# Optimization experiments

Measured on AMD Instinct MI355X. Metric: run time of the kernel, lower is better.

## Reference

```python
import jax, jax.numpy as jnp
import numpy as np


def setup_inputs() -> dict:
    key = jax.random.key(0)
    k0, k1, k2, k3 = jax.random.split(key, 4)
    B, H, W, C, h = 2, 64, 64, 256, 8
    N = H * W
    # per-pixel, per-head (dy, dx) match offsets; a few pixels of displacement
    max_offset = jax.random.normal(k0, (B, N, h, 2), dtype=jnp.float32) * 4.0
    q = jax.random.normal(k1, (B, N, C), dtype=jnp.float32)
    k = jax.random.normal(k2, (B, N, C), dtype=jnp.float32)
    v = jax.random.normal(k3, (B, N, C), dtype=jnp.float32)
    return {"max_offset": max_offset, "q": q, "k": k, "v": v,
            "H": H, "W": W, "r_h": 3, "r_w": 3}


def reference(max_offset, q, k, v, H, W, r_h, r_w):
    """MatchAttention fused forward (l1_norm, scale=1.0).

    Each query pixel (y,x), head g attends to a (2*r_h+1)x(2*r_w+1) window
    centered at (y,x) + round(max_offset[...,g]), clamped to the image.
    Similarity is the negative L1 distance between q and gathered k.
    Returns (output [B,N,C], attn_out [B,N,h,K]).
    """
    B, N, C = q.shape
    h = max_offset.shape[2]
    Ch = C // h
    scale = 1.0
    attn_type = "l1_norm"  # fixed; 'l2_norm' would use squared distance

    # window deltas, K = (2*r_h+1)*(2*r_w+1)
    dy = jnp.arange(-r_h, r_h + 1)
    dx = jnp.arange(-r_w, r_w + 1)
    gy, gx = jnp.meshgrid(dy, dx, indexing="ij")
    ddy, ddx = gy.reshape(-1), gx.reshape(-1)  # [K]

    ys = (jnp.arange(N) // W)[None, :, None]  # [1,N,1]
    xs = (jnp.arange(N) % W)[None, :, None]

    off = jnp.round(max_offset).astype(jnp.int32)  # [B,N,h,2] (dy,dx)
    cy = ys + off[..., 0]                          # [B,N,h] window center
    cx = xs + off[..., 1]
    py = jnp.clip(cy[..., None] + ddy, 0, H - 1)   # [B,N,h,K]
    px = jnp.clip(cx[..., None] + ddx, 0, W - 1)
    idx = py * W + px                              # flat pixel index, [B,N,h,K]

    # split heads and move head axis forward: [B,h,N,Ch]
    qh = q.reshape(B, N, h, Ch).transpose(0, 2, 1, 3)
    kh = k.reshape(B, N, h, Ch).transpose(0, 2, 1, 3)
    vh = v.reshape(B, N, h, Ch).transpose(0, 2, 1, 3)
    idx_t = idx.transpose(0, 2, 1, 3)              # [B,h,N,K]

    # gather windows: [B,h,N,K,Ch]
    gather = jax.vmap(jax.vmap(lambda tbl, i: tbl[i]))
    kg = gather(kh, idx_t)
    vg = gather(vh, idx_t)

    # negative L1 distance similarity, softmax over window
    sim = -scale * jnp.abs(qh[:, :, :, None, :] - kg).sum(-1)  # [B,h,N,K]
    attn = jax.nn.softmax(sim, axis=-1)

    out = jnp.einsum("bhnk,bhnkc->bhnc", attn, vg)
    output = out.transpose(0, 2, 1, 3).reshape(B, N, C)
    attn_out = attn.transpose(0, 2, 1, 3)          # [B,N,h,K]
    return output, attn_out
```

## Files before the change

### kernel.cpp

```cpp
#include <hip/hip_runtime.h>
#include <math.h>

constexpr int B = 2, H = 64, W = 64, C = 256, NH = 8, CH = 32;
constexpr int R = 3, KW = 7, KK = 49, N = H * W;
constexpr int PIX = 32;

template <int CTRL>
static __device__ __forceinline__ float dpp_mov(float v) {
  union { float f; int i; } u;
  u.f = v;
  u.i = __builtin_amdgcn_update_dpp(u.i, u.i, CTRL, 0xf, 0xf, true);
  return u.f;
}
#define DPP_QUAD_XOR1 0xB1
#define DPP_QUAD_XOR2 0x4E
#define DPP_HALF_MIRROR 0x141

__global__ void __launch_bounds__(256) match_attn_kernel(
    const float* __restrict__ moff, const float* __restrict__ qp,
    const float* __restrict__ kp, const float* __restrict__ vp,
    float* __restrict__ outp, float* __restrict__ attnp) {
  const int t = threadIdx.x;
  const int e8 = t & 7;
  const int p = t >> 3;
  const int lbase = (t & 63) & ~7;

  const int xcd = blockIdx.x & 7;
  const int rest = blockIdx.x >> 3;
  const int bg = xcd * 2 + (rest >> 7);
  const int slot = rest & 127;
  const int y = slot >> 1;
  const int x = (slot & 1) * PIX + p;
  const int g = bg & 7;
  const int b = bg >> 3;
  const int n = y * W + x;

  const float2 off = *(const float2*)(moff + ((size_t)(b * N + n) * NH + g) * 2);
  const int cy = y + (int)rintf(off.x);
  const int cx = x + (int)rintf(off.y);

  int pxo[KW], pyo[KW];
#pragma unroll
  for (int i = 0; i < KW; ++i) {
    pxo[i] = min(max(cx + i - R, 0), W - 1) << 10;
    pyo[i] = min(max(cy + i - R, 0), H - 1) * (W << 10);
  }
  const int chn = g * CH + e8 * 4;
  const int cb = chn * 4;
  const char* kimg = (const char*)(kp + (size_t)b * N * C);
  const char* vimg = (const char*)(vp + (size_t)b * N * C);

  const float4 q0 = *(const float4*)(qp + (size_t)(b * N + n) * C + chn);

  float ev[7];
#pragma unroll
  for (int j = 0; j < 7; ++j) ev[j] = 0.f;
  float d = 0.f;
  for (int iy = 0; iy < KW; ++iy) {
    const int rowo = cb + pyo[iy];
#pragma unroll
    for (int ix = 0; ix < KW; ++ix) {
      const float4 k0 = *(const float4*)(kimg + (rowo + pxo[ix]));
      float s = fabsf(q0.x - k0.x) + fabsf(q0.y - k0.y) +
                fabsf(q0.z - k0.z) + fabsf(q0.w - k0.w);
      s += dpp_mov<DPP_QUAD_XOR1>(s);
      s += dpp_mov<DPP_QUAD_XOR2>(s);
      s += dpp_mov<DPP_HALF_MIRROR>(s);
      const float e = __expf(-s);
      d += e;
      const int kk = iy * KW + ix;
      if ((kk & 7) == e8) ev[kk >> 3] = e;
    }
  }
  const float inv = 1.0f / d;

  float* attn_px = attnp + ((size_t)(b * N + n) * NH + g) * KK;
#pragma unroll
  for (int j = 0; j < 7; ++j) {
    const int kk = 8 * j + e8;
    const float w = ev[j] * inv;
    ev[j] = w;
    if (kk < KK) attn_px[kk] = w;
  }

  float4 acc = {0.f, 0.f, 0.f, 0.f};
  for (int iy = 0; iy < KW; ++iy) {
    const int rowo = cb + pyo[iy];
#pragma unroll
    for (int ix = 0; ix < KW; ++ix) {
      const int kk = iy * KW + ix;
      const float w = __shfl(ev[kk >> 3], lbase | (kk & 7), 64);
      const float4 v0 = *(const float4*)(vimg + (rowo + pxo[ix]));
      acc.x += w * v0.x; acc.y += w * v0.y;
      acc.z += w * v0.z; acc.w += w * v0.w;
    }
  }
  *(float4*)(outp + (size_t)(b * N + n) * C + chn) = acc;
}

extern "C" void kernel_launch(void* const* d_in, const int* in_sizes, int n_in,
                              void* d_out, int out_size, void* d_ws, size_t ws_size,
                              hipStream_t stream) {
  const float* moff = (const float*)d_in[0];
  const float* q    = (const float*)d_in[1];
  const float* k    = (const float*)d_in[2];
  const float* v    = (const float*)d_in[3];
  float* out  = (float*)d_out;
  float* attn = out + (size_t)B * N * C;

  const int grid = B * NH * N / PIX;
  match_attn_kernel<<<grid, 256, 0, stream>>>(moff, q, k, v, out, attn);
}
```

Measured before the change: 127.5 us.

## Fuse softmax and V accumulation into single pass with deferred normalization

Merges the two window passes into one: each row's K and V vectors are loaded together and the unnormalized exp weights are accumulated against V right away, with the softmax normalization applied once at the end. This removes the second gather pass over the window and the per-element cross-lane shuffles of the weights. Attention weights are now kept per row by the lane whose index matches the row and written out as 7 contiguous values. Occupancy is pinned with launch_bounds(256,4), and the denominator is split into two partial sums. The change raises register pressure because 14 float4 values are live per row.

```diff
diff --git a/kernel.cpp b/kernel.cpp
--- a/kernel.cpp
+++ b/kernel.cpp
@@ -16,14 +16,13 @@
 #define DPP_QUAD_XOR2 0x4E
 #define DPP_HALF_MIRROR 0x141
 
-__global__ void __launch_bounds__(256) match_attn_kernel(
+__global__ void __launch_bounds__(256, 4) match_attn_kernel(
     const float* __restrict__ moff, const float* __restrict__ qp,
     const float* __restrict__ kp, const float* __restrict__ vp,
     float* __restrict__ outp, float* __restrict__ attnp) {
   const int t = threadIdx.x;
   const int e8 = t & 7;
   const int p = t >> 3;
-  const int lbase = (t & 63) & ~7;
 
   const int xcd = blockIdx.x & 7;
   const int rest = blockIdx.x >> 3;
@@ -52,50 +51,48 @@
 
   const float4 q0 = *(const float4*)(qp + (size_t)(b * N + n) * C + chn);
 
-  float ev[7];
+  float ev7[KW];
 #pragma unroll
-  for (int j = 0; j < 7; ++j) ev[j] = 0.f;
-  float d = 0.f;
+  for (int i = 0; i < KW; ++i) ev7[i] = 0.f;
+  float4 acc = {0.f, 0.f, 0.f, 0.f};
+  float d0 = 0.f, d1 = 0.f;
+
   for (int iy = 0; iy < KW; ++iy) {
     const int rowo = cb + pyo[iy];
+    float4 kr[KW], vr[KW];
+#pragma unroll
+    for (int ix = 0; ix < KW; ++ix)
+      kr[ix] = *(const float4*)(kimg + (rowo + pxo[ix]));
+#pragma unroll
+    for (int ix = 0; ix < KW; ++ix)
+      vr[ix] = *(const float4*)(vimg + (rowo + pxo[ix]));
+
+    const bool own = (iy == e8);
 #pragma unroll
     for (int ix = 0; ix < KW; ++ix) {
-      const float4 k0 = *(const float4*)(kimg + (rowo + pxo[ix]));
-      float s = fabsf(q0.x - k0.x) + fabsf(q0.y - k0.y) +
-                fabsf(q0.z - k0.z) + fabsf(q0.w - k0.w);
+      float s = fabsf(q0.x - kr[ix].x) + fabsf(q0.y - kr[ix].y) +
+                fabsf(q0.z - kr[ix].z) + fabsf(q0.w - kr[ix].w);
       s += dpp_mov<DPP_QUAD_XOR1>(s);
       s += dpp_mov<DPP_QUAD_XOR2>(s);
       s += dpp_mov<DPP_HALF_MIRROR>(s);
       const float e = __expf(-s);
-      d += e;
-      const int kk = iy * KW + ix;
-      if ((kk & 7) == e8) ev[kk >> 3] = e;
+      if (ix & 1) d1 += e; else d0 += e;
+      if (own) ev7[ix] = e;
+      acc.x += e * vr[ix].x; acc.y += e * vr[ix].y;
+      acc.z += e * vr[ix].z; acc.w += e * vr[ix].w;
     }
   }
-  const float inv = 1.0f / d;
+  const float inv = 1.0f / (d0 + d1);
 
-  float* attn_px = attnp + ((size_t)(b * N + n) * NH + g) * KK;
+  float4 o;
+  o.x = acc.x * inv; o.y = acc.y * inv; o.z = acc.z * inv; o.w = acc.w * inv;
+  *(float4*)(outp + (size_t)(b * N + n) * C + chn) = o;
+
+  if (e8 < KW) {
+    float* attn_row = attnp + ((size_t)(b * N + n) * NH + g) * KK + e8 * KW;
 #pragma unroll
-  for (int j = 0; j < 7; ++j) {
-    const int kk = 8 * j + e8;
-    const float w = ev[j] * inv;
-    ev[j] = w;
-    if (kk < KK) attn_px[kk] = w;
+    for (int ix = 0; ix < KW; ++ix) attn_row[ix] = ev7[ix] * inv;
   }
-
-  float4 acc = {0.f, 0.f, 0.f, 0.f};
-  for (int iy = 0; iy < KW; ++iy) {
-    const int rowo = cb + pyo[iy];
-#pragma unroll
-    for (int ix = 0; ix < KW; ++ix) {
-      const int kk = iy * KW + ix;
-      const float w = __shfl(ev[kk >> 3], lbase | (kk & 7), 64);
-      const float4 v0 = *(const float4*)(vimg + (rowo + pxo[ix]));
-      acc.x += w * v0.x; acc.y += w * v0.y;
-      acc.z += w * v0.z; acc.w += w * v0.w;
-    }
-  }
-  *(float4*)(outp + (size_t)(b * N + n) * C + chn) = acc;
 }
 
 extern "C" void kernel_launch(void* const* d_in, const int* in_sizes, int n_in,
```

Result: slower. 168.9 us (+32.5%).
